# Performance work log

Measured on AMD Instinct MI355X. Metric: run time of the kernel, lower is better.

## Reference

```python
import jax, jax.numpy as jnp
import numpy as np

N_DRUG = 50000
N_GENE = 50000
E = 600000
D_IN = 128
D_HID = 64
D_EMB = 32


def setup_inputs() -> dict:
    key = jax.random.key(0)
    ks = jax.random.split(key, 32)
    inp = {}
    inp['x_drug'] = jax.random.normal(ks[0], (N_DRUG, D_IN), jnp.float32)
    inp['x_gene'] = jax.random.normal(ks[1], (N_GENE, D_IN), jnp.float32)
    # per-etype edge lists (src,dst)
    inp['dd_src'] = jax.random.randint(ks[2], (E,), 0, N_DRUG)
    inp['dd_dst'] = jax.random.randint(ks[3], (E,), 0, N_DRUG)
    inp['dg_src'] = jax.random.randint(ks[4], (E,), 0, N_DRUG)
    inp['dg_dst'] = jax.random.randint(ks[5], (E,), 0, N_GENE)
    inp['gd_src'] = jax.random.randint(ks[6], (E,), 0, N_GENE)
    inp['gd_dst'] = jax.random.randint(ks[7], (E,), 0, N_DRUG)
    inp['gg_src'] = jax.random.randint(ks[8], (E,), 0, N_GENE)
    inp['gg_dst'] = jax.random.randint(ks[9], (E,), 0, N_GENE)
    # layer-1 per-relation weights (in -> hidden) and per-ntype biases
    s1 = 1.0 / np.sqrt(D_IN)
    inp['W1_dd'] = jax.random.normal(ks[10], (D_IN, D_HID), jnp.float32) * s1
    inp['W1_dg'] = jax.random.normal(ks[11], (D_IN, D_HID), jnp.float32) * s1
    inp['W1_gd'] = jax.random.normal(ks[12], (D_IN, D_HID), jnp.float32) * s1
    inp['W1_gg'] = jax.random.normal(ks[13], (D_IN, D_HID), jnp.float32) * s1
    inp['b1_drug'] = jnp.zeros((D_HID,), jnp.float32)
    inp['b1_gene'] = jnp.zeros((D_HID,), jnp.float32)
    # layer-2 per-relation weights (hidden -> embed) and per-ntype biases
    s2 = 1.0 / np.sqrt(D_HID)
    inp['W2_dd'] = jax.random.normal(ks[14], (D_HID, D_EMB), jnp.float32) * s2
    inp['W2_dg'] = jax.random.normal(ks[15], (D_HID, D_EMB), jnp.float32) * s2
    inp['W2_gd'] = jax.random.normal(ks[16], (D_HID, D_EMB), jnp.float32) * s2
    inp['W2_gg'] = jax.random.normal(ks[17], (D_HID, D_EMB), jnp.float32) * s2
    inp['b2_drug'] = jnp.zeros((D_EMB,), jnp.float32)
    inp['b2_gene'] = jnp.zeros((D_EMB,), jnp.float32)
    return inp


def _rel_mean(x_src, W, src, dst, n_dst):
    # transform-then-gather (efficient when out_dim <= in_dim), segment-mean over dst
    m = (x_src @ W)[src]                                  # [E, out]
    s = jax.ops.segment_sum(m, dst, num_segments=n_dst)   # [n_dst, out]
    deg = jax.ops.segment_sum(jnp.ones((src.shape[0],), m.dtype), dst, num_segments=n_dst)
    return s / jnp.maximum(deg, 1.0)[:, None]


def _rgcn_layer(xd, xg, Wdd, Wdg, Wgd, Wgg, bd, bg,
                dd_src, dd_dst, dg_src, dg_dst, gd_src, gd_dst, gg_src, gg_dst, act):
    hd = (_rel_mean(xd, Wdd, dd_src, dd_dst, N_DRUG)
          + _rel_mean(xg, Wgd, gd_src, gd_dst, N_DRUG) + bd)
    hg = (_rel_mean(xd, Wdg, dg_src, dg_dst, N_GENE)
          + _rel_mean(xg, Wgg, gg_src, gg_dst, N_GENE) + bg)
    if act:
        hd = jax.nn.relu(hd)
        hg = jax.nn.relu(hg)
    return hd, hg


def reference(x_drug, x_gene, dd_src, dd_dst, dg_src, dg_dst, gd_src, gd_dst,
              gg_src, gg_dst, W1_dd, W1_dg, W1_gd, W1_gg, b1_drug, b1_gene,
              W2_dd, W2_dg, W2_gd, W2_gg, b2_drug, b2_gene):
    hd, hg = _rgcn_layer(x_drug, x_gene, W1_dd, W1_dg, W1_gd, W1_gg, b1_drug, b1_gene,
                         dd_src, dd_dst, dg_src, dg_dst, gd_src, gd_dst, gg_src, gg_dst, True)
    hd, hg = _rgcn_layer(hd, hg, W2_dd, W2_dg, W2_gd, W2_gg, b2_drug, b2_gene,
                         dd_src, dd_dst, dg_src, dg_dst, gd_src, gd_dst, gg_src, gg_dst, False)
    # concatenate per-ntype embeddings: rows [0:N_DRUG]=drug, [N_DRUG:]=gene
    return jnp.concatenate([hd, hg], axis=0)
```

## Files before the change

### kernel.cpp

```cpp
#include <hip/hip_runtime.h>
#include <hip/hip_bf16.h>

#define N_NODE 50000
#define NEDGE  600000
#define NRANGE 128
#define RSZ    391
#define CAPB   6144
#define CHUNK  4096
#define NBLK1  147

typedef __hip_bfloat16 bf16;
typedef __attribute__((ext_vector_type(8))) short short8;
typedef __attribute__((ext_vector_type(4))) float floatx4;

__device__ __forceinline__ short f2s(float f) {
    bf16 t = __float2bfloat16(f);
    return *(short*)&t;
}
__device__ __forceinline__ unsigned pk2(float lo, float hi) {
    return ((unsigned)(unsigned short)f2s(lo)) | (((unsigned)(unsigned short)f2s(hi)) << 16);
}
__device__ __forceinline__ void acc2(float& a, float& b, unsigned w, float m) {
    a += m * __uint_as_float(w << 16);
    b += m * __uint_as_float(w & 0xFFFF0000u);
}


__global__ __launch_bounds__(256) void k_part(
    const int* __restrict__ d0, const int* __restrict__ s0,
    const int* __restrict__ d1, const int* __restrict__ s1,
    const int* __restrict__ d2, const int* __restrict__ s2,
    const int* __restrict__ d3, const int* __restrict__ s3,
    int* __restrict__ gcur, unsigned* __restrict__ gpart)
{
    __shared__ int hcur[NRANGE];
    __shared__ int delta[NRANGE];
    __shared__ int sc[256];
    __shared__ unsigned buf[CHUNK];
    int bid = blockIdx.x;
    int rel = bid / NBLK1;
    int c   = bid - rel * NBLK1;
    int tid = threadIdx.x;
    const int* dp = rel == 0 ? d0 : rel == 1 ? d1 : rel == 2 ? d2 : d3;
    const int* sp = rel == 0 ? s0 : rel == 1 ? s1 : rel == 2 ? s2 : s3;
    int e0 = c * CHUNK;
    int e1 = min(e0 + CHUNK, NEDGE);
    int cnt_chunk = e1 - e0;

    if (tid < NRANGE) hcur[tid] = 0;
    __syncthreads();
    for (int e = e0 + tid; e < e1; e += 256)
        atomicAdd(&hcur[dp[e] / RSZ], 1);
    __syncthreads();
    int v = (tid < NRANGE) ? hcur[tid] : 0;
    sc[tid] = v;
    __syncthreads();
    for (int d = 1; d < NRANGE; d <<= 1) {
        int t = (tid >= d && tid < NRANGE) ? sc[tid - d] : 0;
        __syncthreads();
        sc[tid] += t;
        __syncthreads();
    }
    if (tid < NRANGE) {
        int start = sc[tid] - v;
        int bg    = rel * NRANGE + tid;
        int resv  = atomicAdd(&gcur[bg], v);
        delta[tid] = bg * CAPB + resv - start;
        hcur[tid]  = start;
    }
    __syncthreads();
    for (int e = e0 + tid; e < e1; e += 256) {
        int d = dp[e];
        int b = d / RSZ;
        int p = atomicAdd(&hcur[b], 1);
        buf[p] = ((unsigned)b << 25) | ((unsigned)(d - b * RSZ) << 16) | (unsigned)sp[e];
    }
    __syncthreads();
    for (int i = tid; i < cnt_chunk; i += 256) {
        unsigned key = buf[i];
        gpart[delta[key >> 25] + i] = key;
    }
}

__global__ __launch_bounds__(512) void k_base(
    const int* __restrict__ gcur, int* __restrict__ base_rel)
{
    __shared__ int sc[512];
    int t = threadIdx.x;
    int v = gcur[t];
    sc[t] = v;
    __syncthreads();
    int loc = t & (NRANGE - 1);
    for (int d = 1; d < NRANGE; d <<= 1) {
        int x = (loc >= d) ? sc[t - d] : 0;
        __syncthreads();
        sc[t] += x;
        __syncthreads();
    }
    base_rel[t] = sc[t] - v;
}

__global__ __launch_bounds__(256) void k_csr(
    const unsigned* __restrict__ gpart, const int* __restrict__ gcnt,
    const int* __restrict__ base_rel, int* __restrict__ off, int* __restrict__ edges)
{
    __shared__ int cur[RSZ];
    __shared__ unsigned short stg[CAPB];
    __shared__ int sc[256];
    int bid = blockIdx.x;
    int rel = bid >> 7, r = bid & (NRANGE - 1);
    int tid = threadIdx.x;
    int range0 = r * RSZ;
    int RS = min(RSZ, N_NODE - range0);
    if (RS < 0) RS = 0;
    int count = gcnt[bid];
    int base  = base_rel[bid];
    size_t slot0 = (size_t)bid * CAPB;

    for (int i = tid; i < RSZ; i += 256) cur[i] = 0;
    __syncthreads();
    for (int i = tid; i < count; i += 256)
        atomicAdd(&cur[(gpart[slot0 + i] >> 16) & 0x1FF], 1);
    __syncthreads();
    int vloc[2]; int run = 0;
#pragma unroll
    for (int j = 0; j < 2; j++) {
        int idx = tid * 2 + j;
        int x = (idx < RSZ) ? cur[idx] : 0;
        vloc[j] = x; run += x;
    }
    sc[tid] = run;
    __syncthreads();
    for (int d = 1; d < 256; d <<= 1) {
        int t = (tid >= d) ? sc[tid - d] : 0;
        __syncthreads();
        sc[tid] += t;
        __syncthreads();
    }
    int excl = sc[tid] - run;
    run = excl;
#pragma unroll
    for (int j = 0; j < 2; j++) {
        int idx = tid * 2 + j;
        if (idx < RSZ) { int x = vloc[j]; cur[idx] = run; run += x; }
    }
    __syncthreads();
    for (int i = tid; i < RS; i += 256)
        off[rel * (N_NODE + 1) + range0 + i] = base + cur[i];
    if (r == NRANGE - 1 && tid == 0) off[rel * (N_NODE + 1) + N_NODE] = NEDGE;
    __syncthreads();
    for (int i = tid; i < count; i += 256) {
        unsigned key = gpart[slot0 + i];
        int p = atomicAdd(&cur[(key >> 16) & 0x1FF], 1);
        stg[p] = (unsigned short)(key & 0xFFFFu);
    }
    __syncthreads();
    for (int i = tid; i < count; i += 256)
        edges[rel * NEDGE + base + i] = (int)stg[i];
}

template <int K, int NOUT, bool AFP32>
__global__ __launch_bounds__(256) void k_gemm_pair(
    const void* __restrict__ X0, const void* __restrict__ X1,
    const float* __restrict__ Wa0, const float* __restrict__ Wb0,
    const float* __restrict__ Wa1, const float* __restrict__ Wb1,
    bf16* __restrict__ out0, bf16* __restrict__ out1, int M)
{
    constexpr int NB  = NOUT / 16;
    constexpr int KC  = K / 32;
    constexpr int NH  = NOUT / 2;
    constexpr int NBL = (NB == 8) ? 3 : 2;
    __shared__ short Wl[KC * NB * 512];

    int sel = blockIdx.y;
    const void*  X  = sel ? X1 : X0;
    const float* Wa = sel ? Wa1 : Wa0;
    const float* Wb = sel ? Wb1 : Wb0;
    bf16*        out = sel ? out1 : out0;

    int tid = threadIdx.x;
    for (int i = tid; i < KC * NB * 512; i += 256) {
        int j  = i & 7;
        int n  = (i >> 3) & 15;
        int q  = (i >> 7) & 3;
        int nb = (i >> 9) & (NB - 1);
        int kc = i >> (9 + NBL);
        int k  = kc * 32 + q * 8 + j;
        int c  = nb * 16 + n;
        float w = (c < NH) ? Wa[k * NH + c] : Wb[k * NH + (c - NH)];
        Wl[i] = f2s(w);
    }
    __syncthreads();

    int lane = tid & 63, wv = tid >> 6;
    int q = lane >> 4, lidx = lane & 15;
    int row0 = blockIdx.x * 64 + wv * 16;
    int rowA = min(row0 + lidx, M - 1);

    floatx4 acc[NB];
#pragma unroll
    for (int nb = 0; nb < NB; nb++) acc[nb] = (floatx4){0.f, 0.f, 0.f, 0.f};

#pragma unroll
    for (int kc = 0; kc < KC; kc++) {
        short8 a;
        if constexpr (AFP32) {
            const float* Xf = (const float*)X + (size_t)rowA * K + kc * 32 + q * 8;
            float4 f0 = *(const float4*)Xf;
            float4 f1 = *(const float4*)(Xf + 4);
            a[0] = f2s(f0.x); a[1] = f2s(f0.y); a[2] = f2s(f0.z); a[3] = f2s(f0.w);
            a[4] = f2s(f1.x); a[5] = f2s(f1.y); a[6] = f2s(f1.z); a[7] = f2s(f1.w);
        } else {
            a = *(const short8*)((const short*)X + (size_t)rowA * K + kc * 32 + q * 8);
        }
#pragma unroll
        for (int nb = 0; nb < NB; nb++) {
            short8 b = *(const short8*)&Wl[((kc * NB + nb) * 64 + lane) * 8];
            acc[nb] = __builtin_amdgcn_mfma_f32_16x16x32_bf16(a, b, acc[nb], 0, 0, 0);
        }
    }
#pragma unroll
    for (int nb = 0; nb < NB; nb++) {
#pragma unroll
        for (int r = 0; r < 4; r++) {
            int row = row0 + q * 4 + r;
            if (row < M)
                out[(size_t)row * NOUT + nb * 16 + lidx] = __float2bfloat16(acc[nb][r]);
        }
    }
}

template<int ROWU>
__device__ __forceinline__ void seg_run(
    int n, const int* __restrict__ ep, float sc,
    const unsigned* __restrict__ base, float* s)
{
    int nfull = n & ~3;
    for (int i = 0; i < nfull; i += 4) {
        int e0 = ep[i + 0];
        int e1 = ep[i + 1];
        int e2 = ep[i + 2];
        int e3 = ep[i + 3];
        uint4 w0 = *(const uint4*)(base + e0 * ROWU);
        uint4 w1 = *(const uint4*)(base + e1 * ROWU);
        uint4 w2 = *(const uint4*)(base + e2 * ROWU);
        uint4 w3 = *(const uint4*)(base + e3 * ROWU);
        acc2(s[0], s[1], w0.x, sc); acc2(s[2], s[3], w0.y, sc);
        acc2(s[4], s[5], w0.z, sc); acc2(s[6], s[7], w0.w, sc);
        acc2(s[0], s[1], w1.x, sc); acc2(s[2], s[3], w1.y, sc);
        acc2(s[4], s[5], w1.z, sc); acc2(s[6], s[7], w1.w, sc);
        acc2(s[0], s[1], w2.x, sc); acc2(s[2], s[3], w2.y, sc);
        acc2(s[4], s[5], w2.z, sc); acc2(s[6], s[7], w2.w, sc);
        acc2(s[0], s[1], w3.x, sc); acc2(s[2], s[3], w3.y, sc);
        acc2(s[4], s[5], w3.z, sc); acc2(s[6], s[7], w3.w, sc);
    }
    for (int i = nfull; i < n; i++) {
        int e = ep[i];
        uint4 w = *(const uint4*)(base + e * ROWU);
        acc2(s[0], s[1], w.x, sc); acc2(s[2], s[3], w.y, sc);
        acc2(s[4], s[5], w.z, sc); acc2(s[6], s[7], w.w, sc);
    }
}

__global__ __launch_bounds__(256) void k_gather64v2(
    const bf16* __restrict__ m1,
    const int* __restrict__ offA0, const int* __restrict__ eA0,
    const int* __restrict__ offB0, const int* __restrict__ eB0,
    const float* __restrict__ bias0, bf16* __restrict__ out0,
    const int* __restrict__ offA1, const int* __restrict__ eA1,
    const int* __restrict__ offB1, const int* __restrict__ eB1,
    const float* __restrict__ bias1, bf16* __restrict__ out1)
{
    int tid  = threadIdx.x;
    int gid  = blockIdx.x * 32 + (tid >> 3);
    int lidx = tid & 7;
    int half = (gid >= N_NODE);
    int wid  = gid - (half ? N_NODE : 0);
    const int* offA = half ? offA1 : offA0;
    const int* eA   = half ? eA1   : eA0;
    const int* offB = half ? offB1 : offB0;
    const int* eB   = half ? eB1   : eB0;
    const float* bias = half ? bias1 : bias0;
    bf16* out = half ? out1 : out0;

    const unsigned* base = (const unsigned*)m1 + (half ? 32 : 0) + lidx * 4;

    int begA = offA[wid], nA = offA[wid + 1] - begA;
    int begB = offB[wid], nB = offB[wid + 1] - begB;
    float ia = 1.f / (float)max(nA, 1);
    float ib = 1.f / (float)max(nB, 1);

    float s[8] = {0.f,0.f,0.f,0.f,0.f,0.f,0.f,0.f};
    seg_run<64>(nA, eA + begA, ia, base, s);
    seg_run<64>(nB, eB + begB, ib, base + N_NODE * 64, s);

    float h[8];
#pragma unroll
    for (int k = 0; k < 8; k++)
        h[k] = fmaxf(s[k] + bias[lidx * 8 + k], 0.f);
    uint4 v;
    v.x = pk2(h[0], h[1]); v.y = pk2(h[2], h[3]);
    v.z = pk2(h[4], h[5]); v.w = pk2(h[6], h[7]);
    *(uint4*)(out + (size_t)wid * 64 + lidx * 8) = v;
}

__global__ __launch_bounds__(256) void k_gather32v2(
    const bf16* __restrict__ m2,
    const int* __restrict__ offA0, const int* __restrict__ eA0,
    const int* __restrict__ offB0, const int* __restrict__ eB0,
    const float* __restrict__ bias0, float* __restrict__ out0,
    const int* __restrict__ offA1, const int* __restrict__ eA1,
    const int* __restrict__ offB1, const int* __restrict__ eB1,
    const float* __restrict__ bias1, float* __restrict__ out1)
{
    int tid  = threadIdx.x;
    int gid  = blockIdx.x * 64 + (tid >> 2);
    int lidx = tid & 3;
    if (gid >= 2 * N_NODE) return;
    int half = (gid >= N_NODE);
    int wid  = gid - (half ? N_NODE : 0);
    const int* offA = half ? offA1 : offA0;
    const int* eA   = half ? eA1   : eA0;
    const int* offB = half ? offB1 : offB0;
    const int* eB   = half ? eB1   : eB0;
    const float* bias = half ? bias1 : bias0;
    float* out = half ? out1 : out0;

    const unsigned* base = (const unsigned*)m2 + (half ? 16 : 0) + lidx * 4;

    int begA = offA[wid], nA = offA[wid + 1] - begA;
    int begB = offB[wid], nB = offB[wid + 1] - begB;
    float ia = 1.f / (float)max(nA, 1);
    float ib = 1.f / (float)max(nB, 1);

    float s[8] = {0.f,0.f,0.f,0.f,0.f,0.f,0.f,0.f};
    seg_run<32>(nA, eA + begA, ia, base, s);
    seg_run<32>(nB, eB + begB, ib, base + N_NODE * 32, s);

    float* o = out + (size_t)wid * 32 + lidx * 8;
    float4 v0, v1;
    v0.x = s[0] + bias[lidx * 8 + 0];
    v0.y = s[1] + bias[lidx * 8 + 1];
    v0.z = s[2] + bias[lidx * 8 + 2];
    v0.w = s[3] + bias[lidx * 8 + 3];
    v1.x = s[4] + bias[lidx * 8 + 4];
    v1.y = s[5] + bias[lidx * 8 + 5];
    v1.z = s[6] + bias[lidx * 8 + 6];
    v1.w = s[7] + bias[lidx * 8 + 7];
    *(float4*)o = v0;
    *(float4*)(o + 4) = v1;
}

extern "C" void kernel_launch(void* const* d_in, const int* in_sizes, int n_in,
                              void* d_out, int out_size, void* d_ws, size_t ws_size,
                              hipStream_t stream)
{
    const float* xd = (const float*)d_in[0];
    const float* xg = (const float*)d_in[1];
    const int* dd_src = (const int*)d_in[2];  const int* dd_dst = (const int*)d_in[3];
    const int* dg_src = (const int*)d_in[4];  const int* dg_dst = (const int*)d_in[5];
    const int* gd_src = (const int*)d_in[6];  const int* gd_dst = (const int*)d_in[7];
    const int* gg_src = (const int*)d_in[8];  const int* gg_dst = (const int*)d_in[9];
    const float* W1dd = (const float*)d_in[10];
    const float* W1dg = (const float*)d_in[11];
    const float* W1gd = (const float*)d_in[12];
    const float* W1gg = (const float*)d_in[13];
    const float* b1d  = (const float*)d_in[14];
    const float* b1g  = (const float*)d_in[15];
    const float* W2dd = (const float*)d_in[16];
    const float* W2dg = (const float*)d_in[17];
    const float* W2gd = (const float*)d_in[18];
    const float* W2gg = (const float*)d_in[19];
    const float* b2d  = (const float*)d_in[20];
    const float* b2g  = (const float*)d_in[21];
    float* out = (float*)d_out;

    int* gcur     = (int*)d_ws;
    int* base_rel = gcur + 512;
    int* off      = base_rel + 512;
    int* edges    = off + 4 * (N_NODE + 1);
    bf16* md1     = (bf16*)(edges + 4 * NEDGE);
    bf16* mg1     = md1 + (size_t)N_NODE * 128;
    bf16* hd      = mg1 + (size_t)N_NODE * 128;
    bf16* hg      = hd + (size_t)N_NODE * 64;
    bf16* md2     = md1;
    bf16* mg2     = md1 + (size_t)N_NODE * 64;
    unsigned* gpart = (unsigned*)md1;

    hipMemsetAsync(gcur, 0, 512 * sizeof(int), stream);
    k_part<<<4 * NBLK1, 256, 0, stream>>>(
        dd_dst, dd_src, gd_dst, gd_src, dg_dst, dg_src, gg_dst, gg_src, gcur, gpart);
    k_base<<<1, 512, 0, stream>>>(gcur, base_rel);
    k_csr<<<512, 256, 0, stream>>>(gpart, gcur, base_rel, off, edges);

    const int* off_dd = off + 0 * (N_NODE + 1);
    const int* off_gd = off + 1 * (N_NODE + 1);
    const int* off_dg = off + 2 * (N_NODE + 1);
    const int* off_gg = off + 3 * (N_NODE + 1);
    const int* e_dd = edges + 0 * NEDGE;
    const int* e_gd = edges + 1 * NEDGE;
    const int* e_dg = edges + 2 * NEDGE;
    const int* e_gg = edges + 3 * NEDGE;

    dim3 gemm_grid((N_NODE + 63) / 64, 2);
    int g64_grid = (2 * N_NODE) / 32;
    int g32_grid = (2 * N_NODE + 63) / 64;

    k_gemm_pair<128, 128, true><<<gemm_grid, 256, 0, stream>>>(
        xd, xg, W1dd, W1dg, W1gd, W1gg, md1, mg1, N_NODE);
    k_gather64v2<<<g64_grid, 256, 0, stream>>>(
        md1,
        off_dd, e_dd, off_gd, e_gd, b1d, hd,
        off_dg, e_dg, off_gg, e_gg, b1g, hg);

    k_gemm_pair<64, 64, false><<<gemm_grid, 256, 0, stream>>>(
        hd, hg, W2dd, W2dg, W2gd, W2gg, md2, mg2, N_NODE);
    k_gather32v2<<<g32_grid, 256, 0, stream>>>(
        md2,
        off_dd, e_dd, off_gd, e_gd, b2d, out,
        off_dg, e_dg, off_gg, e_gg, b2g, out + (size_t)N_NODE * 32);
}
```

Baseline: 338.5 us.

## Degree-sort gather nodes, store edges as uint16, fold base scan into CSR

```diff
diff --git a/kernel.cpp b/kernel.cpp
--- a/kernel.cpp
+++ b/kernel.cpp
@@ -82,27 +82,9 @@
     }
 }
 
-__global__ __launch_bounds__(512) void k_base(
-    const int* __restrict__ gcur, int* __restrict__ base_rel)
-{
-    __shared__ int sc[512];
-    int t = threadIdx.x;
-    int v = gcur[t];
-    sc[t] = v;
-    __syncthreads();
-    int loc = t & (NRANGE - 1);
-    for (int d = 1; d < NRANGE; d <<= 1) {
-        int x = (loc >= d) ? sc[t - d] : 0;
-        __syncthreads();
-        sc[t] += x;
-        __syncthreads();
-    }
-    base_rel[t] = sc[t] - v;
-}
-
 __global__ __launch_bounds__(256) void k_csr(
     const unsigned* __restrict__ gpart, const int* __restrict__ gcnt,
-    const int* __restrict__ base_rel, int* __restrict__ off, int* __restrict__ edges)
+    int* __restrict__ off, unsigned short* __restrict__ edges)
 {
     __shared__ int cur[RSZ];
     __shared__ unsigned short stg[CAPB];
@@ -114,8 +96,19 @@
     int RS = min(RSZ, N_NODE - range0);
     if (RS < 0) RS = 0;
     int count = gcnt[bid];
-    int base  = base_rel[bid];
     size_t slot0 = (size_t)bid * CAPB;
+
+    int vb = (tid < NRANGE) ? gcnt[rel * NRANGE + tid] : 0;
+    sc[tid] = vb;
+    __syncthreads();
+    for (int d = 1; d < NRANGE; d <<= 1) {
+        int t = (tid >= d && tid < NRANGE) ? sc[tid - d] : 0;
+        __syncthreads();
+        sc[tid] += t;
+        __syncthreads();
+    }
+    int base = (r > 0) ? sc[r - 1] : 0;
+    __syncthreads();
 
     for (int i = tid; i < RSZ; i += 256) cur[i] = 0;
     __syncthreads();
@@ -156,7 +149,65 @@
     }
     __syncthreads();
     for (int i = tid; i < count; i += 256)
-        edges[rel * NEDGE + base + i] = (int)stg[i];
+        edges[(size_t)rel * NEDGE + base + i] = stg[i];
+}
+
+__global__ __launch_bounds__(512) void k_ohist(
+    const int* __restrict__ off, int* __restrict__ bins)
+{
+    __shared__ int lb[64];
+    int tid = threadIdx.x;
+    if (tid < 64) lb[tid] = 0;
+    __syncthreads();
+    int u = blockIdx.x * 512 + tid;
+    if (u < 2 * N_NODE) {
+        int half = u >= N_NODE;
+        int w = u - (half ? N_NODE : 0);
+        const int* oA = off + (half ? 2 : 0) * (N_NODE + 1);
+        const int* oB = off + (half ? 3 : 1) * (N_NODE + 1);
+        int nT = (oA[w + 1] - oA[w]) + (oB[w + 1] - oB[w]);
+        atomicAdd(&lb[min(nT, 63)], 1);
+    }
+    __syncthreads();
+    if (tid < 64 && lb[tid]) atomicAdd(&bins[tid], lb[tid]);
+}
+
+__global__ void k_oscan(const int* __restrict__ bins, int* __restrict__ cursor)
+{
+    __shared__ int s[64];
+    int t = threadIdx.x;
+    s[t] = bins[t];
+    __syncthreads();
+    int acc = 0;
+    for (int b = t + 1; b < 64; b++) acc += s[b];
+    cursor[t] = acc;
+}
+
+__global__ __launch_bounds__(512) void k_oscat(
+    const int* __restrict__ off, int* __restrict__ cursor, int* __restrict__ order)
+{
+    __shared__ int lb[64], lbase[64], lcur[64];
+    int tid = threadIdx.x;
+    if (tid < 64) { lb[tid] = 0; lcur[tid] = 0; }
+    __syncthreads();
+    int u = blockIdx.x * 512 + tid;
+    int b = -1;
+    if (u < 2 * N_NODE) {
+        int half = u >= N_NODE;
+        int w = u - (half ? N_NODE : 0);
+        const int* oA = off + (half ? 2 : 0) * (N_NODE + 1);
+        const int* oB = off + (half ? 3 : 1) * (N_NODE + 1);
+        int nT = (oA[w + 1] - oA[w]) + (oB[w + 1] - oB[w]);
+        b = min(nT, 63);
+        atomicAdd(&lb[b], 1);
+    }
+    __syncthreads();
+    if (tid < 64 && lb[tid]) lbase[tid] = atomicAdd(&cursor[tid], lb[tid]);
+    __syncthreads();
+    if (b >= 0) {
+        int p = atomicAdd(&lcur[b], 1);
+        order[lbase[b] + p] = u;
+    }
 }
 
 template <int K, int NOUT, bool AFP32>
@@ -232,7 +283,7 @@
 
 template<int ROWU>
 __device__ __forceinline__ void seg_run(
-    int n, const int* __restrict__ ep, float sc,
+    int n, const unsigned short* __restrict__ ep, float sc,
     const unsigned* __restrict__ base, float* s)
 {
     int nfull = n & ~3;
@@ -262,24 +313,25 @@
     }
 }
 
-__global__ __launch_bounds__(256) void k_gather64v2(
-    const bf16* __restrict__ m1,
-    const int* __restrict__ offA0, const int* __restrict__ eA0,
-    const int* __restrict__ offB0, const int* __restrict__ eB0,
+__global__ __launch_bounds__(256) void k_gather64v4(
+    const bf16* __restrict__ m1, const int* __restrict__ order,
+    const int* __restrict__ offA0, const unsigned short* __restrict__ eA0,
+    const int* __restrict__ offB0, const unsigned short* __restrict__ eB0,
     const float* __restrict__ bias0, bf16* __restrict__ out0,
-    const int* __restrict__ offA1, const int* __restrict__ eA1,
-    const int* __restrict__ offB1, const int* __restrict__ eB1,
+    const int* __restrict__ offA1, const unsigned short* __restrict__ eA1,
+    const int* __restrict__ offB1, const unsigned short* __restrict__ eB1,
     const float* __restrict__ bias1, bf16* __restrict__ out1)
 {
     int tid  = threadIdx.x;
     int gid  = blockIdx.x * 32 + (tid >> 3);
     int lidx = tid & 7;
-    int half = (gid >= N_NODE);
-    int wid  = gid - (half ? N_NODE : 0);
+    int u    = order[gid];
+    int half = (u >= N_NODE);
+    int wid  = u - (half ? N_NODE : 0);
     const int* offA = half ? offA1 : offA0;
-    const int* eA   = half ? eA1   : eA0;
+    const unsigned short* eA = half ? eA1 : eA0;
     const int* offB = half ? offB1 : offB0;
-    const int* eB   = half ? eB1   : eB0;
+    const unsigned short* eB = half ? eB1 : eB0;
     const float* bias = half ? bias1 : bias0;
     bf16* out = half ? out1 : out0;
 
@@ -304,25 +356,26 @@
     *(uint4*)(out + (size_t)wid * 64 + lidx * 8) = v;
 }
 
-__global__ __launch_bounds__(256) void k_gather32v2(
-    const bf16* __restrict__ m2,
-    const int* __restrict__ offA0, const int* __restrict__ eA0,
-    const int* __restrict__ offB0, const int* __restrict__ eB0,
+__global__ __launch_bounds__(256) void k_gather32v4(
+    const bf16* __restrict__ m2, const int* __restrict__ order,
+    const int* __restrict__ offA0, const unsigned short* __restrict__ eA0,
+    const int* __restrict__ offB0, const unsigned short* __restrict__ eB0,
     const float* __restrict__ bias0, float* __restrict__ out0,
-    const int* __restrict__ offA1, const int* __restrict__ eA1,
-    const int* __restrict__ offB1, const int* __restrict__ eB1,
+    const int* __restrict__ offA1, const unsigned short* __restrict__ eA1,
+    const int* __restrict__ offB1, const unsigned short* __restrict__ eB1,
     const float* __restrict__ bias1, float* __restrict__ out1)
 {
     int tid  = threadIdx.x;
     int gid  = blockIdx.x * 64 + (tid >> 2);
     int lidx = tid & 3;
     if (gid >= 2 * N_NODE) return;
-    int half = (gid >= N_NODE);
-    int wid  = gid - (half ? N_NODE : 0);
+    int u    = order[gid];
+    int half = (u >= N_NODE);
+    int wid  = u - (half ? N_NODE : 0);
     const int* offA = half ? offA1 : offA0;
-    const int* eA   = half ? eA1   : eA0;
+    const unsigned short* eA = half ? eA1 : eA0;
     const int* offB = half ? offB1 : offB0;
-    const int* eB   = half ? eB1   : eB0;
+    const unsigned short* eB = half ? eB1 : eB0;
     const float* bias = half ? bias1 : bias0;
     float* out = half ? out1 : out0;
 
@@ -376,31 +429,37 @@
     float* out = (float*)d_out;
 
     int* gcur     = (int*)d_ws;
-    int* base_rel = gcur + 512;
-    int* off      = base_rel + 512;
-    int* edges    = off + 4 * (N_NODE + 1);
-    bf16* md1     = (bf16*)(edges + 4 * NEDGE);
+    int* bins     = gcur + 512;
+    int* cursor   = bins + 64;
+    int* off      = gcur + 1024;
+    unsigned short* edges = (unsigned short*)(off + 4 * (N_NODE + 1));
+    bf16* md1     = (bf16*)(edges + (size_t)4 * NEDGE);
     bf16* mg1     = md1 + (size_t)N_NODE * 128;
     bf16* hd      = mg1 + (size_t)N_NODE * 128;
     bf16* hg      = hd + (size_t)N_NODE * 64;
+    int*  order   = (int*)(hg + (size_t)N_NODE * 64);
     bf16* md2     = md1;
     bf16* mg2     = md1 + (size_t)N_NODE * 64;
     unsigned* gpart = (unsigned*)md1;
 
-    hipMemsetAsync(gcur, 0, 512 * sizeof(int), stream);
+    hipMemsetAsync(gcur, 0, 1024 * sizeof(int), stream);
     k_part<<<4 * NBLK1, 256, 0, stream>>>(
         dd_dst, dd_src, gd_dst, gd_src, dg_dst, dg_src, gg_dst, gg_src, gcur, gpart);
-    k_base<<<1, 512, 0, stream>>>(gcur, base_rel);
-    k_csr<<<512, 256, 0, stream>>>(gpart, gcur, base_rel, off, edges);
+    k_csr<<<512, 256, 0, stream>>>(gpart, gcur, off, edges);
+
+    int ogrid = (2 * N_NODE + 511) / 512;
+    k_ohist<<<ogrid, 512, 0, stream>>>(off, bins);
+    k_oscan<<<1, 64, 0, stream>>>(bins, cursor);
+    k_oscat<<<ogrid, 512, 0, stream>>>(off, cursor, order);
 
     const int* off_dd = off + 0 * (N_NODE + 1);
     const int* off_gd = off + 1 * (N_NODE + 1);
     const int* off_dg = off + 2 * (N_NODE + 1);
     const int* off_gg = off + 3 * (N_NODE + 1);
-    const int* e_dd = edges + 0 * NEDGE;
-    const int* e_gd = edges + 1 * NEDGE;
-    const int* e_dg = edges + 2 * NEDGE;
-    const int* e_gg = edges + 3 * NEDGE;
+    const unsigned short* e_dd = edges + (size_t)0 * NEDGE;
+    const unsigned short* e_gd = edges + (size_t)1 * NEDGE;
+    const unsigned short* e_dg = edges + (size_t)2 * NEDGE;
+    const unsigned short* e_gg = edges + (size_t)3 * NEDGE;
 
     dim3 gemm_grid((N_NODE + 63) / 64, 2);
     int g64_grid = (2 * N_NODE) / 32;
@@ -408,15 +467,15 @@
 
     k_gemm_pair<128, 128, true><<<gemm_grid, 256, 0, stream>>>(
         xd, xg, W1dd, W1dg, W1gd, W1gg, md1, mg1, N_NODE);
-    k_gather64v2<<<g64_grid, 256, 0, stream>>>(
-        md1,
+    k_gather64v4<<<g64_grid, 256, 0, stream>>>(
+        md1, order,
         off_dd, e_dd, off_gd, e_gd, b1d, hd,
         off_dg, e_dg, off_gg, e_gg, b1g, hg);
 
     k_gemm_pair<64, 64, false><<<gemm_grid, 256, 0, stream>>>(
         hd, hg, W2dd, W2dg, W2gd, W2gg, md2, mg2, N_NODE);
-    k_gather32v2<<<g32_grid, 256, 0, stream>>>(
-        md2,
+    k_gather32v4<<<g32_grid, 256, 0, stream>>>(
+        md2, order,
         off_dd, e_dd, off_gd, e_gd, b2d, out,
         off_dg, e_dg, off_gg, e_gg, b2g, out + (size_t)N_NODE * 32);
 }
```

Result: slower. 355.9 us (+5.1%).

## Fuse edge partition with layer-1 GEMM, fold base scan into CSR, use 16-bit edges

Applied to the files above, without the earlier changes.

```diff
diff --git a/kernel.cpp b/kernel.cpp
--- a/kernel.cpp
+++ b/kernel.cpp
@@ -8,6 +8,7 @@
 #define CAPB   6144
 #define CHUNK  4096
 #define NBLK1  147
+#define GEMM_GX 391
 
 typedef __hip_bfloat16 bf16;
 typedef __attribute__((ext_vector_type(8))) short short8;
@@ -26,87 +27,144 @@
 }
 
 
-__global__ __launch_bounds__(256) void k_part(
+__global__ __launch_bounds__(512) void k_part_gemm(
     const int* __restrict__ d0, const int* __restrict__ s0,
     const int* __restrict__ d1, const int* __restrict__ s1,
     const int* __restrict__ d2, const int* __restrict__ s2,
     const int* __restrict__ d3, const int* __restrict__ s3,
-    int* __restrict__ gcur, unsigned* __restrict__ gpart)
-{
-    __shared__ int hcur[NRANGE];
-    __shared__ int delta[NRANGE];
-    __shared__ int sc[256];
-    __shared__ unsigned buf[CHUNK];
-    int bid = blockIdx.x;
-    int rel = bid / NBLK1;
-    int c   = bid - rel * NBLK1;
+    int* __restrict__ gcur, unsigned* __restrict__ gpart,
+    const float* __restrict__ X0, const float* __restrict__ X1,
+    const float* __restrict__ Wa0, const float* __restrict__ Wb0,
+    const float* __restrict__ Wa1, const float* __restrict__ Wb1,
+    bf16* __restrict__ out0, bf16* __restrict__ out1)
+{
+    __shared__ union {
+        struct { unsigned buf[CHUNK]; int sc[512]; int hcur[NRANGE]; int delta[NRANGE]; } p;
+        short wl[4 * 8 * 512];
+    } u;
+
     int tid = threadIdx.x;
-    const int* dp = rel == 0 ? d0 : rel == 1 ? d1 : rel == 2 ? d2 : d3;
-    const int* sp = rel == 0 ? s0 : rel == 1 ? s1 : rel == 2 ? s2 : s3;
-    int e0 = c * CHUNK;
-    int e1 = min(e0 + CHUNK, NEDGE);
-    int cnt_chunk = e1 - e0;
-
-    if (tid < NRANGE) hcur[tid] = 0;
-    __syncthreads();
-    for (int e = e0 + tid; e < e1; e += 256)
-        atomicAdd(&hcur[dp[e] / RSZ], 1);
-    __syncthreads();
-    int v = (tid < NRANGE) ? hcur[tid] : 0;
-    sc[tid] = v;
-    __syncthreads();
-    for (int d = 1; d < NRANGE; d <<= 1) {
-        int t = (tid >= d && tid < NRANGE) ? sc[tid - d] : 0;
-        __syncthreads();
-        sc[tid] += t;
-        __syncthreads();
-    }
-    if (tid < NRANGE) {
-        int start = sc[tid] - v;
-        int bg    = rel * NRANGE + tid;
-        int resv  = atomicAdd(&gcur[bg], v);
-        delta[tid] = bg * CAPB + resv - start;
-        hcur[tid]  = start;
-    }
-    __syncthreads();
-    for (int e = e0 + tid; e < e1; e += 256) {
-        int d = dp[e];
-        int b = d / RSZ;
-        int p = atomicAdd(&hcur[b], 1);
-        buf[p] = ((unsigned)b << 25) | ((unsigned)(d - b * RSZ) << 16) | (unsigned)sp[e];
-    }
-    __syncthreads();
-    for (int i = tid; i < cnt_chunk; i += 256) {
-        unsigned key = buf[i];
-        gpart[delta[key >> 25] + i] = key;
-    }
-}
-
-__global__ __launch_bounds__(512) void k_base(
-    const int* __restrict__ gcur, int* __restrict__ base_rel)
-{
+    if (blockIdx.x < 4 * NBLK1) {
+        int bid = blockIdx.x;
+        int rel = bid / NBLK1;
+        int c   = bid - rel * NBLK1;
+        const int* dp = rel == 0 ? d0 : rel == 1 ? d1 : rel == 2 ? d2 : d3;
+        const int* sp = rel == 0 ? s0 : rel == 1 ? s1 : rel == 2 ? s2 : s3;
+        int e0 = c * CHUNK;
+        int e1 = min(e0 + CHUNK, NEDGE);
+        int cnt = e1 - e0;
+        const int4* dp4 = (const int4*)(dp + e0);
+        const int4* sp4 = (const int4*)(sp + e0);
+        int nv = cnt >> 2;
+
+        if (tid < NRANGE) u.p.hcur[tid] = 0;
+        __syncthreads();
+        for (int i = tid; i < nv; i += 512) {
+            int4 d = dp4[i];
+            atomicAdd(&u.p.hcur[d.x / RSZ], 1);
+            atomicAdd(&u.p.hcur[d.y / RSZ], 1);
+            atomicAdd(&u.p.hcur[d.z / RSZ], 1);
+            atomicAdd(&u.p.hcur[d.w / RSZ], 1);
+        }
+        __syncthreads();
+        int v = (tid < NRANGE) ? u.p.hcur[tid] : 0;
+        u.p.sc[tid] = v;
+        __syncthreads();
+        for (int d = 1; d < NRANGE; d <<= 1) {
+            int t = (tid >= d && tid < NRANGE) ? u.p.sc[tid - d] : 0;
+            __syncthreads();
+            if (tid < NRANGE) u.p.sc[tid] += t;
+            __syncthreads();
+        }
+        if (tid < NRANGE) {
+            int start = u.p.sc[tid] - v;
+            int bg    = rel * NRANGE + tid;
+            int resv  = atomicAdd(&gcur[bg], v);
+            u.p.delta[tid] = bg * CAPB + resv - start;
+            u.p.hcur[tid]  = start;
+        }
+        __syncthreads();
+        for (int i = tid; i < nv; i += 512) {
+            int4 d = dp4[i];
+            int4 s = sp4[i];
+#define PUT(dd, ss) { int b = (dd) / RSZ; int p = atomicAdd(&u.p.hcur[b], 1); \
+                      u.p.buf[p] = ((unsigned)b << 25) | ((unsigned)((dd) - b * RSZ) << 16) | (unsigned)(ss); }
+            PUT(d.x, s.x) PUT(d.y, s.y) PUT(d.z, s.z) PUT(d.w, s.w)
+#undef PUT
+        }
+        __syncthreads();
+        for (int i = tid * 4; i < cnt; i += 2048) {
+            uint4 kb = *(const uint4*)&u.p.buf[i];
+            gpart[u.p.delta[kb.x >> 25] + i + 0] = kb.x;
+            gpart[u.p.delta[kb.y >> 25] + i + 1] = kb.y;
+            gpart[u.p.delta[kb.z >> 25] + i + 2] = kb.z;
+            gpart[u.p.delta[kb.w >> 25] + i + 3] = kb.w;
+        }
+    } else {
+        constexpr int NB = 8, KC = 4, NH = 64;
+        int bid2 = blockIdx.x - 4 * NBLK1;
+        int sel  = bid2 >= GEMM_GX;
+        int bx   = sel ? bid2 - GEMM_GX : bid2;
+        const float* X  = sel ? X1 : X0;
+        const float* Wa = sel ? Wa1 : Wa0;
+        const float* Wb = sel ? Wb1 : Wb0;
+        bf16*       outp = sel ? out1 : out0;
+
+        for (int i = tid; i < KC * NB * 512; i += 512) {
+            int j  = i & 7;
+            int n  = (i >> 3) & 15;
+            int q  = (i >> 7) & 3;
+            int nb = (i >> 9) & (NB - 1);
+            int kc = i >> 12;
+            int k  = kc * 32 + q * 8 + j;
+            int c  = nb * 16 + n;
+            float w = (c < NH) ? Wa[k * NH + c] : Wb[k * NH + (c - NH)];
+            u.wl[i] = f2s(w);
+        }
+        __syncthreads();
+
+        int lane = tid & 63, wv = tid >> 6;
+        int q = lane >> 4, lidx = lane & 15;
+        int row0 = bx * 128 + wv * 16;
+        int rowA = min(row0 + lidx, N_NODE - 1);
+
+        floatx4 acc[NB];
+#pragma unroll
+        for (int nb = 0; nb < NB; nb++) acc[nb] = (floatx4){0.f, 0.f, 0.f, 0.f};
+
+#pragma unroll
+        for (int kc = 0; kc < KC; kc++) {
+            const float* Xf = X + (size_t)rowA * 128 + kc * 32 + q * 8;
+            float4 f0 = *(const float4*)Xf;
+            float4 f1 = *(const float4*)(Xf + 4);
+            short8 a;
+            a[0] = f2s(f0.x); a[1] = f2s(f0.y); a[2] = f2s(f0.z); a[3] = f2s(f0.w);
+            a[4] = f2s(f1.x); a[5] = f2s(f1.y); a[6] = f2s(f1.z); a[7] = f2s(f1.w);
+#pragma unroll
+            for (int nb = 0; nb < NB; nb++) {
+                short8 b = *(const short8*)&u.wl[((kc * NB + nb) * 64 + lane) * 8];
+                acc[nb] = __builtin_amdgcn_mfma_f32_16x16x32_bf16(a, b, acc[nb], 0, 0, 0);
+            }
+        }
+#pragma unroll
+        for (int nb = 0; nb < NB; nb++) {
+#pragma unroll
+            for (int r = 0; r < 4; r++) {
+                int row = row0 + q * 4 + r;
+                if (row < N_NODE)
+                    outp[(size_t)row * 128 + nb * 16 + lidx] = __float2bfloat16(acc[nb][r]);
+            }
+        }
+    }
+}
+
+__global__ __launch_bounds__(512) void k_csr(
+    const unsigned* __restrict__ gpart, const int* __restrict__ gcnt,
+    int* __restrict__ off, unsigned short* __restrict__ edges)
+{
+    __shared__ unsigned short stg[CAPB];
+    __shared__ int cur[RSZ];
     __shared__ int sc[512];
-    int t = threadIdx.x;
-    int v = gcur[t];
-    sc[t] = v;
-    __syncthreads();
-    int loc = t & (NRANGE - 1);
-    for (int d = 1; d < NRANGE; d <<= 1) {
-        int x = (loc >= d) ? sc[t - d] : 0;
-        __syncthreads();
-        sc[t] += x;
-        __syncthreads();
-    }
-    base_rel[t] = sc[t] - v;
-}
-
-__global__ __launch_bounds__(256) void k_csr(
-    const unsigned* __restrict__ gpart, const int* __restrict__ gcnt,
-    const int* __restrict__ base_rel, int* __restrict__ off, int* __restrict__ edges)
-{
-    __shared__ int cur[RSZ];
-    __shared__ unsigned short stg[CAPB];
-    __shared__ int sc[256];
     int bid = blockIdx.x;
     int rel = bid >> 7, r = bid & (NRANGE - 1);
     int tid = threadIdx.x;
@@ -114,49 +172,65 @@
     int RS = min(RSZ, N_NODE - range0);
     if (RS < 0) RS = 0;
     int count = gcnt[bid];
-    int base  = base_rel[bid];
-    size_t slot0 = (size_t)bid * CAPB;
-
-    for (int i = tid; i < RSZ; i += 256) cur[i] = 0;
-    __syncthreads();
-    for (int i = tid; i < count; i += 256)
-        atomicAdd(&cur[(gpart[slot0 + i] >> 16) & 0x1FF], 1);
-    __syncthreads();
-    int vloc[2]; int run = 0;
-#pragma unroll
-    for (int j = 0; j < 2; j++) {
-        int idx = tid * 2 + j;
-        int x = (idx < RSZ) ? cur[idx] : 0;
-        vloc[j] = x; run += x;
-    }
-    sc[tid] = run;
-    __syncthreads();
-    for (int d = 1; d < 256; d <<= 1) {
+    const uint4* gp4 = (const uint4*)(gpart + (size_t)bid * CAPB);
+    const unsigned* gp = gpart + (size_t)bid * CAPB;
+    int count4 = count & ~3;
+
+    int vb = (tid < NRANGE) ? gcnt[rel * NRANGE + tid] : 0;
+    sc[tid] = vb;
+    __syncthreads();
+    for (int d = 1; d < NRANGE; d <<= 1) {
+        int t = (tid >= d && tid < NRANGE) ? sc[tid - d] : 0;
+        __syncthreads();
+        if (tid < NRANGE) sc[tid] += t;
+        __syncthreads();
+    }
+    int base = (r > 0) ? sc[r - 1] : 0;
+    __syncthreads();
+
+    for (int i = tid; i < RSZ; i += 512) cur[i] = 0;
+    __syncthreads();
+    for (int i = tid * 4; i < count4; i += 2048) {
+        uint4 g = gp4[i >> 2];
+        atomicAdd(&cur[(g.x >> 16) & 0x1FF], 1);
+        atomicAdd(&cur[(g.y >> 16) & 0x1FF], 1);
+        atomicAdd(&cur[(g.z >> 16) & 0x1FF], 1);
+        atomicAdd(&cur[(g.w >> 16) & 0x1FF], 1);
+    }
+    if (tid < (count & 3))
+        atomicAdd(&cur[(gp[count4 + tid] >> 16) & 0x1FF], 1);
+    __syncthreads();
+    int x = (tid < RSZ) ? cur[tid] : 0;
+    sc[tid] = x;
+    __syncthreads();
+    for (int d = 1; d < 512; d <<= 1) {
         int t = (tid >= d) ? sc[tid - d] : 0;
         __syncthreads();
         sc[tid] += t;
         __syncthreads();
     }
-    int excl = sc[tid] - run;
-    run = excl;
-#pragma unroll
-    for (int j = 0; j < 2; j++) {
-        int idx = tid * 2 + j;
-        if (idx < RSZ) { int x = vloc[j]; cur[idx] = run; run += x; }
-    }
-    __syncthreads();
-    for (int i = tid; i < RS; i += 256)
+    int excl = sc[tid] - x;
+    __syncthreads();
+    if (tid < RSZ) cur[tid] = excl;
+    __syncthreads();
+    for (int i = tid; i < RS; i += 512)
         off[rel * (N_NODE + 1) + range0 + i] = base + cur[i];
     if (r == NRANGE - 1 && tid == 0) off[rel * (N_NODE + 1) + N_NODE] = NEDGE;
     __syncthreads();
-    for (int i = tid; i < count; i += 256) {
-        unsigned key = gpart[slot0 + i];
-        int p = atomicAdd(&cur[(key >> 16) & 0x1FF], 1);
-        stg[p] = (unsigned short)(key & 0xFFFFu);
-    }
-    __syncthreads();
-    for (int i = tid; i < count; i += 256)
-        edges[rel * NEDGE + base + i] = (int)stg[i];
+    for (int i = tid * 4; i < count4; i += 2048) {
+        uint4 g = gp4[i >> 2];
+#define SCAT(gg) { int p = atomicAdd(&cur[((gg) >> 16) & 0x1FF], 1); stg[p] = (unsigned short)((gg) & 0xFFFFu); }
+        SCAT(g.x) SCAT(g.y) SCAT(g.z) SCAT(g.w)
+#undef SCAT
+    }
+    if (tid < (count & 3)) {
+        unsigned g = gp[count4 + tid];
+        int p = atomicAdd(&cur[(g >> 16) & 0x1FF], 1);
+        stg[p] = (unsigned short)(g & 0xFFFFu);
+    }
+    __syncthreads();
+    for (int i = tid; i < count; i += 512)
+        edges[(size_t)rel * NEDGE + base + i] = stg[i];
 }
 
 template <int K, int NOUT, bool AFP32>
@@ -232,7 +306,7 @@
 
 template<int ROWU>
 __device__ __forceinline__ void seg_run(
-    int n, const int* __restrict__ ep, float sc,
+    int n, const unsigned short* __restrict__ ep, float sc,
     const unsigned* __restrict__ base, float* s)
 {
     int nfull = n & ~3;
@@ -262,13 +336,13 @@
     }
 }
 
-__global__ __launch_bounds__(256) void k_gather64v2(
+__global__ __launch_bounds__(256) void k_gather64v5(
     const bf16* __restrict__ m1,
-    const int* __restrict__ offA0, const int* __restrict__ eA0,
-    const int* __restrict__ offB0, const int* __restrict__ eB0,
+    const int* __restrict__ offA0, const unsigned short* __restrict__ eA0,
+    const int* __restrict__ offB0, const unsigned short* __restrict__ eB0,
     const float* __restrict__ bias0, bf16* __restrict__ out0,
-    const int* __restrict__ offA1, const int* __restrict__ eA1,
-    const int* __restrict__ offB1, const int* __restrict__ eB1,
+    const int* __restrict__ offA1, const unsigned short* __restrict__ eA1,
+    const int* __restrict__ offB1, const unsigned short* __restrict__ eB1,
     const float* __restrict__ bias1, bf16* __restrict__ out1)
 {
     int tid  = threadIdx.x;
@@ -277,9 +351,9 @@
     int half = (gid >= N_NODE);
     int wid  = gid - (half ? N_NODE : 0);
     const int* offA = half ? offA1 : offA0;
-    const int* eA   = half ? eA1   : eA0;
+    const unsigned short* eA = half ? eA1 : eA0;
     const int* offB = half ? offB1 : offB0;
-    const int* eB   = half ? eB1   : eB0;
+    const unsigned short* eB = half ? eB1 : eB0;
     const float* bias = half ? bias1 : bias0;
     bf16* out = half ? out1 : out0;
 
@@ -306,11 +380,11 @@
 
 __global__ __launch_bounds__(256) void k_gather32v2(
     const bf16* __restrict__ m2,
-    const int* __restrict__ offA0, const int* __restrict__ eA0,
-    const int* __restrict__ offB0, const int* __restrict__ eB0,
+    const int* __restrict__ offA0, const unsigned short* __restrict__ eA0,
+    const int* __restrict__ offB0, const unsigned short* __restrict__ eB0,
     const float* __restrict__ bias0, float* __restrict__ out0,
-    const int* __restrict__ offA1, const int* __restrict__ eA1,
-    const int* __restrict__ offB1, const int* __restrict__ eB1,
+    const int* __restrict__ offA1, const unsigned short* __restrict__ eA1,
+    const int* __restrict__ offB1, const unsigned short* __restrict__ eB1,
     const float* __restrict__ bias1, float* __restrict__ out1)
 {
     int tid  = threadIdx.x;
@@ -320,9 +394,9 @@
     int half = (gid >= N_NODE);
     int wid  = gid - (half ? N_NODE : 0);
     const int* offA = half ? offA1 : offA0;
-    const int* eA   = half ? eA1   : eA0;
+    const unsigned short* eA = half ? eA1 : eA0;
     const int* offB = half ? offB1 : offB0;
-    const int* eB   = half ? eB1   : eB0;
+    const unsigned short* eB = half ? eB1 : eB0;
     const float* bias = half ? bias1 : bias0;
     float* out = half ? out1 : out0;
 
@@ -376,45 +450,45 @@
     float* out = (float*)d_out;
 
     int* gcur     = (int*)d_ws;
-    int* base_rel = gcur + 512;
-    int* off      = base_rel + 512;
-    int* edges    = off + 4 * (N_NODE + 1);
-    bf16* md1     = (bf16*)(edges + 4 * NEDGE);
+    int* off      = gcur + 512;
+    unsigned short* edges = (unsigned short*)(off + 4 * (N_NODE + 1));
+    bf16* md1     = (bf16*)(edges + (size_t)4 * NEDGE);
     bf16* mg1     = md1 + (size_t)N_NODE * 128;
-    bf16* hd      = mg1 + (size_t)N_NODE * 128;
-    bf16* hg      = hd + (size_t)N_NODE * 64;
+    bf16* h       = mg1 + (size_t)N_NODE * 128;
+    bf16* hd      = h;
+    bf16* hg      = h + (size_t)N_NODE * 64;
     bf16* md2     = md1;
     bf16* mg2     = md1 + (size_t)N_NODE * 64;
-    unsigned* gpart = (unsigned*)md1;
+    unsigned* gpart = (unsigned*)h;
 
     hipMemsetAsync(gcur, 0, 512 * sizeof(int), stream);
-    k_part<<<4 * NBLK1, 256, 0, stream>>>(
-        dd_dst, dd_src, gd_dst, gd_src, dg_dst, dg_src, gg_dst, gg_src, gcur, gpart);
-    k_base<<<1, 512, 0, stream>>>(gcur, base_rel);
-    k_csr<<<512, 256, 0, stream>>>(gpart, gcur, base_rel, off, edges);
+    k_part_gemm<<<4 * NBLK1 + 2 * GEMM_GX, 512, 0, stream>>>(
+        dd_dst, dd_src, gd_dst, gd_src, dg_dst, dg_src, gg_dst, gg_src, gcur, gpart,
+        xd, xg, W1dd, W1dg, W1gd, W1gg, md1, mg1);
+
+    k_csr<<<512, 512, 0, stream>>>(gpart, gcur, off, edges);
 
     const int* off_dd = off + 0 * (N_NODE + 1);
     const int* off_gd = off + 1 * (N_NODE + 1);
     const int* off_dg = off + 2 * (N_NODE + 1);
     const int* off_gg = off + 3 * (N_NODE + 1);
-    const int* e_dd = edges + 0 * NEDGE;
-    const int* e_gd = edges + 1 * NEDGE;
-    const int* e_dg = edges + 2 * NEDGE;
-    const int* e_gg = edges + 3 * NEDGE;
-
-    dim3 gemm_grid((N_NODE + 63) / 64, 2);
+    const unsigned short* e_dd = edges + (size_t)0 * NEDGE;
+    const unsigned short* e_gd = edges + (size_t)1 * NEDGE;
+    const unsigned short* e_dg = edges + (size_t)2 * NEDGE;
+    const unsigned short* e_gg = edges + (size_t)3 * NEDGE;
+
     int g64_grid = (2 * N_NODE) / 32;
     int g32_grid = (2 * N_NODE + 63) / 64;
-
-    k_gemm_pair<128, 128, true><<<gemm_grid, 256, 0, stream>>>(
-        xd, xg, W1dd, W1dg, W1gd, W1gg, md1, mg1, N_NODE);
-    k_gather64v2<<<g64_grid, 256, 0, stream>>>(
+    dim3 gemm2_grid((N_NODE + 63) / 64, 2);
+
+    k_gather64v5<<<g64_grid, 256, 0, stream>>>(
         md1,
         off_dd, e_dd, off_gd, e_gd, b1d, hd,
         off_dg, e_dg, off_gg, e_gg, b1g, hg);
 
-    k_gemm_pair<64, 64, false><<<gemm_grid, 256, 0, stream>>>(
+    k_gemm_pair<64, 64, false><<<gemm2_grid, 256, 0, stream>>>(
         hd, hg, W2dd, W2dg, W2gd, W2gg, md2, mg2, N_NODE);
+
     k_gather32v2<<<g32_grid, 256, 0, stream>>>(
         md2,
         off_dd, e_dd, off_gd, e_gd, b2d, out,
```

New measurement: 295.9 us. 1.14x faster.
